# Kernel tuning notes

Hardware: AMD Instinct MI355X
Metric: run time of the kernel (lower is better)

Reference implementation:

```python
import jax, jax.numpy as jnp
import numpy as np

D_MODEL = 768
N_HEADS = 12
HEAD_DIM = D_MODEL // N_HEADS


def setup_inputs() -> dict:
    key = jax.random.key(0)
    ks = jax.random.split(key, 9)
    B, S = 4, 2048
    std = 1.0 / np.sqrt(D_MODEL)
    x = jax.random.normal(ks[0], (B, S, D_MODEL), dtype=jnp.float32)
    Wq = jax.random.normal(ks[1], (D_MODEL, D_MODEL), dtype=jnp.float32) * std
    bq = jnp.zeros((D_MODEL,), dtype=jnp.float32)
    Wk = jax.random.normal(ks[2], (D_MODEL, D_MODEL), dtype=jnp.float32) * std
    bk = jnp.zeros((D_MODEL,), dtype=jnp.float32)
    Wv = jax.random.normal(ks[3], (D_MODEL, D_MODEL), dtype=jnp.float32) * std
    bv = jnp.zeros((D_MODEL,), dtype=jnp.float32)
    Wo = jax.random.normal(ks[4], (D_MODEL, D_MODEL), dtype=jnp.float32) * std
    bo = jnp.zeros((D_MODEL,), dtype=jnp.float32)
    return {"x": x, "Wq": Wq, "bq": bq, "Wk": Wk, "bk": bk,
            "Wv": Wv, "bv": bv, "Wo": Wo, "bo": bo}


def reference(x, Wq, bq, Wk, bk, Wv, bv, Wo, bo):
    B, S, D = x.shape
    H, Hd = N_HEADS, HEAD_DIM
    # QKV projections (torch Linear: y = x @ W^T + b; here W stored as [in,out])
    q = (x @ Wq + bq).reshape(B, S, H, Hd).transpose(0, 2, 1, 3)  # [B,H,S,Hd]
    k = (x @ Wk + bk).reshape(B, S, H, Hd).transpose(0, 2, 1, 3)
    v = (x @ Wv + bv).reshape(B, S, H, Hd).transpose(0, 2, 1, 3)
    scale = 1.0 / jnp.sqrt(jnp.asarray(Hd, dtype=x.dtype))
    scores = jnp.einsum('bhqd,bhkd->bhqk', q, k) * scale  # [B,H,S,S]
    causal = jnp.tril(jnp.ones((S, S), dtype=bool))
    scores = jnp.where(causal, scores, -jnp.inf)
    attn = jax.nn.softmax(scores, axis=-1)
    ctx = jnp.einsum('bhqk,bhkd->bhqd', attn, v)  # [B,H,S,Hd]
    ctx = ctx.transpose(0, 2, 1, 3).reshape(B, S, D)
    return ctx @ Wo + bo
```

## Files before the change

### kernel.cpp

```cpp
#include <hip/hip_runtime.h>
#include <stdint.h>

#define DM    768
#define NH    12
#define HD    64
#define BATCH 4
#define SEQ   2048
#define NTOK  (BATCH*SEQ)
#define NKT   12

typedef unsigned int   u32;
typedef unsigned short u16;
using bf16x8 = __attribute__((ext_vector_type(8))) short;
using f32x4  = __attribute__((ext_vector_type(4))) float;

#define QSCALE 0.18033688011112042f

__device__ __forceinline__ u16 f2bf(float f) {
    u32 u = __float_as_uint(f);
    u = (u + 0x7FFFu + ((u >> 16) & 1u)) >> 16;
    return (u16)u;
}

__device__ __forceinline__ u32 pkbf(float a, float b) {
    u32 r;
    asm("v_cvt_pk_bf16_f32 %0, %1, %2" : "=v"(r) : "v"(a), "v"(b));
    return r;
}

template <int N>
__device__ __forceinline__ void waitvm() {
    if constexpr (N == 0)      asm volatile("s_waitcnt vmcnt(0)" ::: "memory");
    else if constexpr (N == 2) asm volatile("s_waitcnt vmcnt(2)" ::: "memory");
    else if constexpr (N == 4) asm volatile("s_waitcnt vmcnt(4)" ::: "memory");
    else if constexpr (N == 5) asm volatile("s_waitcnt vmcnt(5)" ::: "memory");
    else if constexpr (N == 8) asm volatile("s_waitcnt vmcnt(8)" ::: "memory");
    else if constexpr (N == 9) asm volatile("s_waitcnt vmcnt(9)" ::: "memory");
    else static_assert(N == 0 || N == 2 || N == 4 || N == 5 || N == 8 || N == 9, "add literal");
}

__device__ __forceinline__ void gload_lds16(const void* gptr, void* ldsptr) {
    __builtin_amdgcn_global_load_lds(
        (__attribute__((address_space(1))) const u32*)gptr,
        (__attribute__((address_space(3))) u32*)ldsptr, 16, 0, 0);
}

__device__ __forceinline__ float vmax4(f32x4 v) {
    return fmaxf(fmaxf(v[0], v[1]), fmaxf(v[2], v[3]));
}

__global__ void cvt_x(const float* __restrict__ x, u16* __restrict__ xb, int n4) {
    int i = blockIdx.x * blockDim.x + threadIdx.x;
    if (i >= n4) return;
    float4 v = ((const float4*)x)[i];
    ushort4 o;
    o.x = f2bf(v.x); o.y = f2bf(v.y); o.z = f2bf(v.z); o.w = f2bf(v.w);
    ((ushort4*)xb)[i] = o;
}

__global__ void transpose_w4(const float* __restrict__ q, const float* __restrict__ k,
                             const float* __restrict__ v, const float* __restrict__ o,
                             u16* __restrict__ Wt, u16* __restrict__ Wto) {
    __shared__ float tile[32][33];
    int z = blockIdx.z;
    const float* W = (z == 0) ? q : (z == 1) ? k : (z == 2) ? v : o;
    u16* D = (z < 3) ? (Wt + (size_t)z * DM * DM) : Wto;
    int tx = threadIdx.x, ty = threadIdx.y;
    int x0 = blockIdx.x * 32, y0 = blockIdx.y * 32;
    #pragma unroll
    for (int i = 0; i < 32; i += 8)
        tile[ty + i][tx] = W[(size_t)(y0 + ty + i) * DM + x0 + tx];
    __syncthreads();
    #pragma unroll
    for (int i = 0; i < 32; i += 8)
        D[(size_t)(x0 + ty + i) * DM + y0 + tx] = f2bf(tile[tx][ty + i]);
}

template <int MODE>
__global__ __launch_bounds__(512, 2)
void gemm_pipe(const u16* __restrict__ A, const u16* __restrict__ Bt,
               const float* __restrict__ b0, const float* __restrict__ b1,
               const float* __restrict__ b2,
               u16* __restrict__ Qo, u16* __restrict__ Ko, u16* __restrict__ Vto,
               float* __restrict__ Out)
{
    constexpr int BM = (MODE == 0) ? 256 : 128;
    constexpr int BN = (MODE == 0) ? 288 : 192;
    constexpr int MF = 4;
    constexpr int NF = (MODE == 0) ? 9 : 3;
    constexpr int AL = BM / 64;
    constexpr int BFULL = (MODE == 0) ? 4 : 3;

    __shared__ u16 As[2][BM][64];
    __shared__ u16 Bs[2][BN][64];

    const int t = threadIdx.x;
    const int w = t >> 6, l = t & 63;
    const int l15 = l & 15, lg = l >> 4;
    const int m0 = blockIdx.x * BM;
    const int n0 = blockIdx.y * BN;
    const int waveM = ((MODE == 0) ? (w >> 1) : (w >> 2)) * 64;
    const int waveN = (MODE == 0) ? (w & 1) * 144 : (w & 3) * 48;

    f32x4 zf = {0.f, 0.f, 0.f, 0.f};
    f32x4 acc[MF][NF];
    #pragma unroll
    for (int i = 0; i < MF; ++i)
        #pragma unroll
        for (int j = 0; j < NF; ++j) acc[i][j] = zf;

    const u16* Arow0 = A  + (size_t)m0 * DM;
    const u16* Brow0 = Bt + (size_t)n0 * DM;

    auto stage = [&](int d, int k0) {
        #pragma unroll
        for (int i = 0; i < AL; ++i) {
            int f = i * 512 + t;
            int row = f >> 3, c = f & 7;
            int gc = c ^ (row & 7);
            gload_lds16(Arow0 + (size_t)row * DM + k0 + gc * 8, &As[d][row][c * 8]);
        }
        #pragma unroll
        for (int i = 0; i < BFULL; ++i) {
            int f = i * 512 + t;
            int row = f >> 3, c = f & 7;
            int gc = c ^ (row & 7);
            gload_lds16(Brow0 + (size_t)row * DM + k0 + gc * 8, &Bs[d][row][c * 8]);
        }
        if constexpr (MODE == 0) {
            if (t < 256) {
                int f = 2048 + t;
                int row = f >> 3, c = f & 7;
                int gc = c ^ (row & 7);
                gload_lds16(Brow0 + (size_t)row * DM + k0 + gc * 8, &Bs[d][row][c * 8]);
            }
        }
    };
    auto wait_tile = [&]() {
        if constexpr (MODE == 0) {
            if (w < 4) waitvm<9>(); else waitvm<8>();
        } else {
            waitvm<5>();
        }
    };
    auto phase = [&](int d, int kk) {
        const int ch = ((kk * 4 + lg) ^ (l15 & 7)) * 8;
        bf16x8 af[MF], bfr[NF];
        #pragma unroll
        for (int m = 0; m < MF; ++m)
            af[m] = *(const bf16x8*)&As[d][waveM + m * 16 + l15][ch];
        #pragma unroll
        for (int n = 0; n < NF; ++n)
            bfr[n] = *(const bf16x8*)&Bs[d][waveN + n * 16 + l15][ch];
        __builtin_amdgcn_s_setprio(1);
        #pragma unroll
        for (int m = 0; m < MF; ++m)
            #pragma unroll
            for (int n = 0; n < NF; ++n)
                acc[m][n] = __builtin_amdgcn_mfma_f32_16x16x32_bf16(af[m], bfr[n], acc[m][n], 0, 0, 0);
        __builtin_amdgcn_s_setprio(0);
    };

    stage(0, 0);
    stage(1, 64);

    for (int tt = 0; tt < NKT - 1; ++tt) {
        const int c = tt & 1;
        wait_tile();
        __builtin_amdgcn_s_barrier();
        __builtin_amdgcn_sched_barrier(0);
        phase(c, 0);
        phase(c, 1);
        __builtin_amdgcn_sched_barrier(0);
        __builtin_amdgcn_s_barrier();
        __builtin_amdgcn_sched_barrier(0);
        if (tt + 2 < NKT) stage(c, (tt + 2) * 64);
    }
    {
        waitvm<0>();
        __builtin_amdgcn_s_barrier();
        __builtin_amdgcn_sched_barrier(0);
        phase((NKT - 1) & 1, 0);
        phase((NKT - 1) & 1, 1);
    }

    if (MODE == 1) {
        #pragma unroll
        for (int m = 0; m < MF; ++m) {
            int grow = m0 + waveM + m * 16 + lg * 4;
            #pragma unroll
            for (int n = 0; n < NF; ++n) {
                int gcol = n0 + waveN + n * 16 + l15;
                float bias = b0[gcol];
                #pragma unroll
                for (int r = 0; r < 4; ++r)
                    Out[(size_t)(grow + r) * DM + gcol] = acc[m][n][r] + bias;
            }
        }
    } else {
        #pragma unroll
        for (int m = 0; m < MF; ++m) {
            int grow = m0 + waveM + m * 16 + lg * 4;
            int bb = grow >> 11, ss = grow & 2047;
            #pragma unroll
            for (int n = 0; n < NF; ++n) {
                int nstart = n0 + waveN + n * 16;
                int which = nstart / DM;
                int cbase = nstart - which * DM + l15;
                int h = cbase >> 6, hd = cbase & 63;
                if (which == 0) {
                    float bias = b0[cbase];
                    #pragma unroll
                    for (int r = 0; r < 4; ++r)
                        Qo[(((size_t)bb * NH + h) * SEQ + (ss + r)) * HD + hd] =
                            f2bf((acc[m][n][r] + bias) * QSCALE);
                } else if (which == 1) {
                    float bias = b1[cbase];
                    #pragma unroll
                    for (int r = 0; r < 4; ++r)
                        Ko[(((size_t)bb * NH + h) * SEQ + (ss + r)) * HD + hd] =
                            f2bf(acc[m][n][r] + bias);
                } else {
                    float bias = b2[cbase];
                    u32 lo = pkbf(acc[m][n][0] + bias, acc[m][n][1] + bias);
                    u32 hi = pkbf(acc[m][n][2] + bias, acc[m][n][3] + bias);
                    *(int2*)&Vto[(((size_t)bb * NH + h) * HD + hd) * SEQ + ss] =
                        make_int2((int)lo, (int)hi);
                }
            }
        }
    }
}

__global__ __launch_bounds__(512, 4)
void attn_fwd(const u16* __restrict__ Q, const u16* __restrict__ K_,
              const u16* __restrict__ Vt, u16* __restrict__ ctx)
{
    __shared__ u16 Ks[2][64][64];
    __shared__ u16 Vs[2][64][64];

    const int t = threadIdx.x, w = t >> 6, l = t & 63;
    const int l15 = l & 15, lg = l >> 4;
    const int sw = l15 & 7;
    const int bx = blockIdx.x;
    const int ord = bx / 48;
    const int bh  = bx - ord * 48;
    const int q16 = 15 - ord;
    const int b = bh / NH, h = bh - b * NH;
    const int wrow0 = q16 * 128 + w * 16;
    const int niter = 2 * q16 + 2;

    const u16* Qp = Q + ((size_t)bh * SEQ + wrow0 + l15) * HD;
    bf16x8 qf0 = *(const bf16x8*)(Qp + lg * 8);
    bf16x8 qf1 = *(const bf16x8*)(Qp + 32 + lg * 8);

    f32x4 zf = {0.f, 0.f, 0.f, 0.f};
    f32x4 acc[4];
    #pragma unroll
    for (int d = 0; d < 4; ++d) acc[d] = zf;
    float mi = -INFINITY, li = 0.f;

    const u16* Kbh = K_ + (size_t)bh * SEQ * HD;
    const u16* Vbh = Vt + (size_t)bh * HD * SEQ;

    auto stage = [&](int d, int j0) {
        int row = t >> 3, c = t & 7;
        int gc = (c ^ (row & 7)) * 8;
        gload_lds16(Kbh + (size_t)(j0 + row) * HD + gc, (u16*)Ks[d] + (size_t)t * 8);
        gload_lds16(Vbh + (size_t)row * SEQ + j0 + gc,  (u16*)Vs[d] + (size_t)t * 8);
    };

    stage(0, 0);
    stage(1, 64);

    for (int jt = 0; jt < niter; ++jt) {
        const int cur = jt & 1;
        const int j0 = jt << 6;
        if (jt < niter - 1) waitvm<2>(); else waitvm<0>();
        __builtin_amdgcn_s_barrier();
        __builtin_amdgcn_sched_barrier(0);
        if (j0 <= wrow0 + 15) {
            const u16 (*Kc)[64] = Ks[cur];
            const u16 (*Vc)[64] = Vs[cur];
            f32x4 s0[4];
            __builtin_amdgcn_s_setprio(1);
            #pragma unroll
            for (int nt = 0; nt < 4; ++nt) {
                const u16* krow = Kc[nt * 16 + l15];
                bf16x8 kf0 = *(const bf16x8*)&krow[(lg ^ sw) * 8];
                bf16x8 kf1 = *(const bf16x8*)&krow[((4 + lg) ^ sw) * 8];
                f32x4 a = zf;
                a = __builtin_amdgcn_mfma_f32_16x16x32_bf16(kf0, qf0, a, 0, 0, 0);
                a = __builtin_amdgcn_mfma_f32_16x16x32_bf16(kf1, qf1, a, 0, 0, 0);
                s0[nt] = a;
            }
            __builtin_amdgcn_s_setprio(0);
            if (j0 + 63 > wrow0) {
                #pragma unroll
                for (int nt = 0; nt < 4; ++nt) {
                    int kb = j0 + nt * 16 + lg * 4;
                    #pragma unroll
                    for (int r = 0; r < 4; ++r)
                        if (kb + r > wrow0 + l15) s0[nt][r] = -INFINITY;
                }
            }
            float pm = fmaxf(fmaxf(vmax4(s0[0]), vmax4(s0[1])), fmaxf(vmax4(s0[2]), vmax4(s0[3])));
            pm = fmaxf(pm, __shfl_xor(pm, 16));
            pm = fmaxf(pm, __shfl_xor(pm, 32));
            if (!__all(pm <= mi + 8.f)) {
                float mn = fmaxf(mi, pm);
                float so = __builtin_amdgcn_exp2f(mi - mn);
                mi = mn;
                li *= so;
                float a0 = __shfl(so, lg * 4 + 0), a1 = __shfl(so, lg * 4 + 1);
                float a2 = __shfl(so, lg * 4 + 2), a3 = __shfl(so, lg * 4 + 3);
                #pragma unroll
                for (int d = 0; d < 4; ++d) {
                    acc[d][0] *= a0; acc[d][1] *= a1;
                    acc[d][2] *= a2; acc[d][3] *= a3;
                }
            }
            u32 dwa[8];
            float rs = 0.f;
            #pragma unroll
            for (int nt = 0; nt < 4; ++nt) {
                float p0 = __builtin_amdgcn_exp2f(s0[nt][0] - mi);
                float p1 = __builtin_amdgcn_exp2f(s0[nt][1] - mi);
                float p2 = __builtin_amdgcn_exp2f(s0[nt][2] - mi);
                float p3 = __builtin_amdgcn_exp2f(s0[nt][3] - mi);
                rs += (p0 + p1) + (p2 + p3);
                dwa[nt * 2] = pkbf(p0, p1); dwa[nt * 2 + 1] = pkbf(p2, p3);
            }
            rs += __shfl_xor(rs, 16);
            rs += __shfl_xor(rs, 32);
            li += rs;
            bf16x8 pa0 = __builtin_bit_cast(bf16x8, make_int4((int)dwa[0], (int)dwa[1], (int)dwa[2], (int)dwa[3]));
            bf16x8 pa1 = __builtin_bit_cast(bf16x8, make_int4((int)dwa[4], (int)dwa[5], (int)dwa[6], (int)dwa[7]));
            const int o4 = (lg & 1) * 4, c0 = lg >> 1;
            __builtin_amdgcn_s_setprio(1);
            #pragma unroll
            for (int d = 0; d < 4; ++d) {
                const u16* vrow = Vc[d * 16 + l15];
                int2 v0 = *(const int2*)(vrow + (((c0 + 0) ^ sw) * 8 + o4));
                int2 v1 = *(const int2*)(vrow + (((c0 + 2) ^ sw) * 8 + o4));
                int2 v2 = *(const int2*)(vrow + (((c0 + 4) ^ sw) * 8 + o4));
                int2 v3 = *(const int2*)(vrow + (((c0 + 6) ^ sw) * 8 + o4));
                bf16x8 vf0 = __builtin_bit_cast(bf16x8, make_int4(v0.x, v0.y, v1.x, v1.y));
                bf16x8 vf1 = __builtin_bit_cast(bf16x8, make_int4(v2.x, v2.y, v3.x, v3.y));
                acc[d] = __builtin_amdgcn_mfma_f32_16x16x32_bf16(pa0, vf0, acc[d], 0, 0, 0);
                acc[d] = __builtin_amdgcn_mfma_f32_16x16x32_bf16(pa1, vf1, acc[d], 0, 0, 0);
            }
            __builtin_amdgcn_s_setprio(0);
        }
        if (jt < niter - 1) {
            __builtin_amdgcn_s_barrier();
            __builtin_amdgcn_sched_barrier(0);
            if (jt + 2 < niter) stage(cur, (jt + 2) << 6);
        }
    }

    float e0 = 1.0f / __shfl(li, lg * 4 + 0), e1 = 1.0f / __shfl(li, lg * 4 + 1);
    float e2 = 1.0f / __shfl(li, lg * 4 + 2), e3 = 1.0f / __shfl(li, lg * 4 + 3);
    #pragma unroll
    for (int r = 0; r < 4; ++r) {
        float f0 = (r == 0) ? e0 : (r == 1) ? e1 : (r == 2) ? e2 : e3;
        int s = wrow0 + lg * 4 + r;
        size_t base = ((size_t)b * SEQ + s) * DM + h * HD;
        #pragma unroll
        for (int d = 0; d < 4; ++d)
            ctx[base + d * 16 + l15] = f2bf(acc[d][r] * f0);
    }
}

extern "C" void kernel_launch(void* const* d_in, const int* in_sizes, int n_in,
                              void* d_out, int out_size, void* d_ws, size_t ws_size,
                              hipStream_t stream) {
    const float* x  = (const float*)d_in[0];
    const float* Wq = (const float*)d_in[1];
    const float* bq = (const float*)d_in[2];
    const float* Wk = (const float*)d_in[3];
    const float* bk = (const float*)d_in[4];
    const float* Wv = (const float*)d_in[5];
    const float* bv = (const float*)d_in[6];
    const float* Wo = (const float*)d_in[7];
    const float* bo = (const float*)d_in[8];
    float* out = (float*)d_out;

    char* ws = (char*)d_ws;
    u16* xb  = (u16*)(ws);
    u16* Wt  = (u16*)(ws + 12582912);
    u16* Wto = (u16*)(ws + 16121856);
    u16* Qw  = (u16*)(ws + 17301504);
    u16* Kw  = (u16*)(ws + 29884416);
    u16* Vtw = (u16*)(ws + 42467328);
    u16* ctx = (u16*)(ws + 55050240);

    cvt_x<<<6144, 256, 0, stream>>>(x, xb, NTOK * DM / 4);
    dim3 tb(32, 8), tg4(24, 24, 4);
    transpose_w4<<<tg4, tb, 0, stream>>>(Wq, Wk, Wv, Wo, Wt, Wto);

    dim3 g2(32, 8);
    gemm_pipe<0><<<g2, 512, 0, stream>>>(xb, Wt, bq, bk, bv, Qw, Kw, Vtw, nullptr);
    attn_fwd<<<768, 512, 0, stream>>>(Qw, Kw, Vtw, ctx);
    dim3 g4(64, 4);
    gemm_pipe<1><<<g4, 512, 0, stream>>>(ctx, Wto, bo, nullptr, nullptr, nullptr, nullptr, nullptr, out);
}
```

Before: 124.9 us.

## Pair long and short causal query strips per block for load balance

Measured after the change: 124.8 us. Within noise of the previous version (-0.1%).

```diff
diff --git a/kernel.cpp b/kernel.cpp
--- a/kernel.cpp
+++ b/kernel.cpp
@@ -31,12 +31,11 @@
 template <int N>
 __device__ __forceinline__ void waitvm() {
     if constexpr (N == 0)      asm volatile("s_waitcnt vmcnt(0)" ::: "memory");
-    else if constexpr (N == 2) asm volatile("s_waitcnt vmcnt(2)" ::: "memory");
     else if constexpr (N == 4) asm volatile("s_waitcnt vmcnt(4)" ::: "memory");
     else if constexpr (N == 5) asm volatile("s_waitcnt vmcnt(5)" ::: "memory");
     else if constexpr (N == 8) asm volatile("s_waitcnt vmcnt(8)" ::: "memory");
     else if constexpr (N == 9) asm volatile("s_waitcnt vmcnt(9)" ::: "memory");
-    else static_assert(N == 0 || N == 2 || N == 4 || N == 5 || N == 8 || N == 9, "add literal");
+    else static_assert(N == 0 || N == 4 || N == 5 || N == 8 || N == 9, "add literal");
 }
 
 __device__ __forceinline__ void gload_lds16(const void* gptr, void* ldsptr) {
@@ -232,9 +231,8 @@
     }
 }
 
-__global__ __launch_bounds__(512, 4)
-void attn_fwd(const u16* __restrict__ Q, const u16* __restrict__ K_,
-              const u16* __restrict__ Vt, u16* __restrict__ ctx)
+__global__ void attn_fwd(const u16* __restrict__ Q, const u16* __restrict__ K_,
+                         const u16* __restrict__ Vt, u16* __restrict__ ctx)
 {
     __shared__ u16 Ks[2][64][64];
     __shared__ u16 Vs[2][64][64];
@@ -245,29 +243,113 @@
     const int bx = blockIdx.x;
     const int ord = bx / 48;
     const int bh  = bx - ord * 48;
-    const int q16 = 15 - ord;
+    const int qL = 31 - ord;
+    const int qS = ord;
     const int b = bh / NH, h = bh - b * NH;
-    const int wrow0 = q16 * 128 + w * 16;
-    const int niter = 2 * q16 + 2;
-
-    const u16* Qp = Q + ((size_t)bh * SEQ + wrow0 + l15) * HD;
-    bf16x8 qf0 = *(const bf16x8*)(Qp + lg * 8);
-    bf16x8 qf1 = *(const bf16x8*)(Qp + 32 + lg * 8);
+    const int wrowA = qL * 64 + w * 16;
+    const int wrowB = qS * 64 + w * 16;
+    const int niter = qL + 1;
+
+    const u16* QpA = Q + ((size_t)bh * SEQ + wrowA + l15) * HD;
+    const u16* QpB = Q + ((size_t)bh * SEQ + wrowB + l15) * HD;
+    bf16x8 qA0 = *(const bf16x8*)(QpA + lg * 8);
+    bf16x8 qA1 = *(const bf16x8*)(QpA + 32 + lg * 8);
+    bf16x8 qB0 = *(const bf16x8*)(QpB + lg * 8);
+    bf16x8 qB1 = *(const bf16x8*)(QpB + 32 + lg * 8);
 
     f32x4 zf = {0.f, 0.f, 0.f, 0.f};
-    f32x4 acc[4];
+    f32x4 accA[4], accB[4];
     #pragma unroll
-    for (int d = 0; d < 4; ++d) acc[d] = zf;
-    float mi = -INFINITY, li = 0.f;
+    for (int d = 0; d < 4; ++d) { accA[d] = zf; accB[d] = zf; }
+    float miA = -INFINITY, liA = 0.f;
+    float miB = -INFINITY, liB = 0.f;
 
     const u16* Kbh = K_ + (size_t)bh * SEQ * HD;
     const u16* Vbh = Vt + (size_t)bh * HD * SEQ;
 
     auto stage = [&](int d, int j0) {
-        int row = t >> 3, c = t & 7;
-        int gc = (c ^ (row & 7)) * 8;
-        gload_lds16(Kbh + (size_t)(j0 + row) * HD + gc, (u16*)Ks[d] + (size_t)t * 8);
-        gload_lds16(Vbh + (size_t)row * SEQ + j0 + gc,  (u16*)Vs[d] + (size_t)t * 8);
+        #pragma unroll
+        for (int i = 0; i < 2; ++i) {
+            int f = i * 256 + t;
+            int row = f >> 3, c = f & 7;
+            int gc = (c ^ (row & 7)) * 8;
+            gload_lds16(Kbh + (size_t)(j0 + row) * HD + gc, (u16*)Ks[d] + (size_t)f * 8);
+            gload_lds16(Vbh + (size_t)row * SEQ + j0 + gc,  (u16*)Vs[d] + (size_t)f * 8);
+        }
+    };
+
+    auto strip = [&](const bf16x8& q0, const bf16x8& q1, float& mi, float& li,
+                     f32x4 (&acc)[4], int wrow, bool diag,
+                     const u16 (*Kc)[64], const u16 (*Vc)[64], int j0) {
+        f32x4 s0[4];
+        __builtin_amdgcn_s_setprio(1);
+        #pragma unroll
+        for (int nt = 0; nt < 4; ++nt) {
+            const u16* krow = Kc[nt * 16 + l15];
+            bf16x8 kf0 = *(const bf16x8*)&krow[(lg ^ sw) * 8];
+            bf16x8 kf1 = *(const bf16x8*)&krow[((4 + lg) ^ sw) * 8];
+            f32x4 a = zf;
+            a = __builtin_amdgcn_mfma_f32_16x16x32_bf16(kf0, q0, a, 0, 0, 0);
+            a = __builtin_amdgcn_mfma_f32_16x16x32_bf16(kf1, q1, a, 0, 0, 0);
+            s0[nt] = a;
+        }
+        __builtin_amdgcn_s_setprio(0);
+        if (diag) {
+            #pragma unroll
+            for (int nt = 0; nt < 4; ++nt) {
+                int kb = j0 + nt * 16 + lg * 4;
+                #pragma unroll
+                for (int r = 0; r < 4; ++r)
+                    if (kb + r > wrow + l15) s0[nt][r] = -INFINITY;
+            }
+        }
+        float pm = fmaxf(fmaxf(vmax4(s0[0]), vmax4(s0[1])), fmaxf(vmax4(s0[2]), vmax4(s0[3])));
+        pm = fmaxf(pm, __shfl_xor(pm, 16));
+        pm = fmaxf(pm, __shfl_xor(pm, 32));
+        if (!__all(pm <= mi + 8.f)) {
+            float mn = fmaxf(mi, pm);
+            float so = __builtin_amdgcn_exp2f(mi - mn);
+            mi = mn;
+            li *= so;
+            float a0 = __shfl(so, lg * 4 + 0), a1 = __shfl(so, lg * 4 + 1);
+            float a2 = __shfl(so, lg * 4 + 2), a3 = __shfl(so, lg * 4 + 3);
+            #pragma unroll
+            for (int d = 0; d < 4; ++d) {
+                acc[d][0] *= a0; acc[d][1] *= a1;
+                acc[d][2] *= a2; acc[d][3] *= a3;
+            }
+        }
+        u32 dwa[8];
+        float rs = 0.f;
+        #pragma unroll
+        for (int nt = 0; nt < 4; ++nt) {
+            float p0 = __builtin_amdgcn_exp2f(s0[nt][0] - mi);
+            float p1 = __builtin_amdgcn_exp2f(s0[nt][1] - mi);
+            float p2 = __builtin_amdgcn_exp2f(s0[nt][2] - mi);
+            float p3 = __builtin_amdgcn_exp2f(s0[nt][3] - mi);
+            rs += (p0 + p1) + (p2 + p3);
+            dwa[nt * 2] = pkbf(p0, p1); dwa[nt * 2 + 1] = pkbf(p2, p3);
+        }
+        rs += __shfl_xor(rs, 16);
+        rs += __shfl_xor(rs, 32);
+        li += rs;
+        bf16x8 pa0 = __builtin_bit_cast(bf16x8, make_int4((int)dwa[0], (int)dwa[1], (int)dwa[2], (int)dwa[3]));
+        bf16x8 pa1 = __builtin_bit_cast(bf16x8, make_int4((int)dwa[4], (int)dwa[5], (int)dwa[6], (int)dwa[7]));
+        const int o4 = (lg & 1) * 4, c0 = lg >> 1;
+        __builtin_amdgcn_s_setprio(1);
+        #pragma unroll
+        for (int d = 0; d < 4; ++d) {
+            const u16* vrow = Vc[d * 16 + l15];
+            int2 v0 = *(const int2*)(vrow + (((c0 + 0) ^ sw) * 8 + o4));
+            int2 v1 = *(const int2*)(vrow + (((c0 + 2) ^ sw) * 8 + o4));
+            int2 v2 = *(const int2*)(vrow + (((c0 + 4) ^ sw) * 8 + o4));
+            int2 v3 = *(const int2*)(vrow + (((c0 + 6) ^ sw) * 8 + o4));
+            bf16x8 vf0 = __builtin_bit_cast(bf16x8, make_int4(v0.x, v0.y, v1.x, v1.y));
+            bf16x8 vf1 = __builtin_bit_cast(bf16x8, make_int4(v2.x, v2.y, v3.x, v3.y));
+            acc[d] = __builtin_amdgcn_mfma_f32_16x16x32_bf16(pa0, vf0, acc[d], 0, 0, 0);
+            acc[d] = __builtin_amdgcn_mfma_f32_16x16x32_bf16(pa1, vf1, acc[d], 0, 0, 0);
+        }
+        __builtin_amdgcn_s_setprio(0);
     };
 
     stage(0, 0);
@@ -276,82 +358,12 @@
     for (int jt = 0; jt < niter; ++jt) {
         const int cur = jt & 1;
         const int j0 = jt << 6;
-        if (jt < niter - 1) waitvm<2>(); else waitvm<0>();
+        if (jt < niter - 1) waitvm<4>(); else waitvm<0>();
         __builtin_amdgcn_s_barrier();
         __builtin_amdgcn_sched_barrier(0);
-        if (j0 <= wrow0 + 15) {
-            const u16 (*Kc)[64] = Ks[cur];
-            const u16 (*Vc)[64] = Vs[cur];
-            f32x4 s0[4];
-            __builtin_amdgcn_s_setprio(1);
-            #pragma unroll
-            for (int nt = 0; nt < 4; ++nt) {
-                const u16* krow = Kc[nt * 16 + l15];
-                bf16x8 kf0 = *(const bf16x8*)&krow[(lg ^ sw) * 8];
-                bf16x8 kf1 = *(const bf16x8*)&krow[((4 + lg) ^ sw) * 8];
-                f32x4 a = zf;
-                a = __builtin_amdgcn_mfma_f32_16x16x32_bf16(kf0, qf0, a, 0, 0, 0);
-                a = __builtin_amdgcn_mfma_f32_16x16x32_bf16(kf1, qf1, a, 0, 0, 0);
-                s0[nt] = a;
-            }
-            __builtin_amdgcn_s_setprio(0);
-            if (j0 + 63 > wrow0) {
-                #pragma unroll
-                for (int nt = 0; nt < 4; ++nt) {
-                    int kb = j0 + nt * 16 + lg * 4;
-                    #pragma unroll
-                    for (int r = 0; r < 4; ++r)
-                        if (kb + r > wrow0 + l15) s0[nt][r] = -INFINITY;
-                }
-            }
-            float pm = fmaxf(fmaxf(vmax4(s0[0]), vmax4(s0[1])), fmaxf(vmax4(s0[2]), vmax4(s0[3])));
-            pm = fmaxf(pm, __shfl_xor(pm, 16));
-            pm = fmaxf(pm, __shfl_xor(pm, 32));
-            if (!__all(pm <= mi + 8.f)) {
-                float mn = fmaxf(mi, pm);
-                float so = __builtin_amdgcn_exp2f(mi - mn);
-                mi = mn;
-                li *= so;
-                float a0 = __shfl(so, lg * 4 + 0), a1 = __shfl(so, lg * 4 + 1);
-                float a2 = __shfl(so, lg * 4 + 2), a3 = __shfl(so, lg * 4 + 3);
-                #pragma unroll
-                for (int d = 0; d < 4; ++d) {
-                    acc[d][0] *= a0; acc[d][1] *= a1;
-                    acc[d][2] *= a2; acc[d][3] *= a3;
-                }
-            }
-            u32 dwa[8];
-            float rs = 0.f;
-            #pragma unroll
-            for (int nt = 0; nt < 4; ++nt) {
-                float p0 = __builtin_amdgcn_exp2f(s0[nt][0] - mi);
-                float p1 = __builtin_amdgcn_exp2f(s0[nt][1] - mi);
-                float p2 = __builtin_amdgcn_exp2f(s0[nt][2] - mi);
-                float p3 = __builtin_amdgcn_exp2f(s0[nt][3] - mi);
-                rs += (p0 + p1) + (p2 + p3);
-                dwa[nt * 2] = pkbf(p0, p1); dwa[nt * 2 + 1] = pkbf(p2, p3);
-            }
-            rs += __shfl_xor(rs, 16);
-            rs += __shfl_xor(rs, 32);
-            li += rs;
-            bf16x8 pa0 = __builtin_bit_cast(bf16x8, make_int4((int)dwa[0], (int)dwa[1], (int)dwa[2], (int)dwa[3]));
-            bf16x8 pa1 = __builtin_bit_cast(bf16x8, make_int4((int)dwa[4], (int)dwa[5], (int)dwa[6], (int)dwa[7]));
-            const int o4 = (lg & 1) * 4, c0 = lg >> 1;
-            __builtin_amdgcn_s_setprio(1);
-            #pragma unroll
-            for (int d = 0; d < 4; ++d) {
-                const u16* vrow = Vc[d * 16 + l15];
-                int2 v0 = *(const int2*)(vrow + (((c0 + 0) ^ sw) * 8 + o4));
-                int2 v1 = *(const int2*)(vrow + (((c0 + 2) ^ sw) * 8 + o4));
-                int2 v2 = *(const int2*)(vrow + (((c0 + 4) ^ sw) * 8 + o4));
-                int2 v3 = *(const int2*)(vrow + (((c0 + 6) ^ sw) * 8 + o4));
-                bf16x8 vf0 = __builtin_bit_cast(bf16x8, make_int4(v0.x, v0.y, v1.x, v1.y));
-                bf16x8 vf1 = __builtin_bit_cast(bf16x8, make_int4(v2.x, v2.y, v3.x, v3.y));
-                acc[d] = __builtin_amdgcn_mfma_f32_16x16x32_bf16(pa0, vf0, acc[d], 0, 0, 0);
-                acc[d] = __builtin_amdgcn_mfma_f32_16x16x32_bf16(pa1, vf1, acc[d], 0, 0, 0);
-            }
-            __builtin_amdgcn_s_setprio(0);
-        }
+        strip(qA0, qA1, miA, liA, accA, wrowA, jt == qL, Ks[cur], Vs[cur], j0);
+        if (jt <= qS)
+            strip(qB0, qB1, miB, liB, accB, wrowB, jt == qS, Ks[cur], Vs[cur], j0);
         if (jt < niter - 1) {
             __builtin_amdgcn_s_barrier();
             __builtin_amdgcn_sched_barrier(0);
@@ -359,17 +371,21 @@
         }
     }
 
-    float e0 = 1.0f / __shfl(li, lg * 4 + 0), e1 = 1.0f / __shfl(li, lg * 4 + 1);
-    float e2 = 1.0f / __shfl(li, lg * 4 + 2), e3 = 1.0f / __shfl(li, lg * 4 + 3);
-    #pragma unroll
-    for (int r = 0; r < 4; ++r) {
-        float f0 = (r == 0) ? e0 : (r == 1) ? e1 : (r == 2) ? e2 : e3;
-        int s = wrow0 + lg * 4 + r;
-        size_t base = ((size_t)b * SEQ + s) * DM + h * HD;
-        #pragma unroll
-        for (int d = 0; d < 4; ++d)
-            ctx[base + d * 16 + l15] = f2bf(acc[d][r] * f0);
-    }
+    auto epi = [&](float li, f32x4 (&acc)[4], int wrow) {
+        float e0 = 1.0f / __shfl(li, lg * 4 + 0), e1 = 1.0f / __shfl(li, lg * 4 + 1);
+        float e2 = 1.0f / __shfl(li, lg * 4 + 2), e3 = 1.0f / __shfl(li, lg * 4 + 3);
+        #pragma unroll
+        for (int r = 0; r < 4; ++r) {
+            float f0 = (r == 0) ? e0 : (r == 1) ? e1 : (r == 2) ? e2 : e3;
+            int s = wrow + lg * 4 + r;
+            size_t base = ((size_t)b * SEQ + s) * DM + h * HD;
+            #pragma unroll
+            for (int d = 0; d < 4; ++d)
+                ctx[base + d * 16 + l15] = f2bf(acc[d][r] * f0);
+        }
+    };
+    epi(liA, accA, wrowA);
+    epi(liB, accB, wrowB);
 }
 
 extern "C" void kernel_launch(void* const* d_in, const int* in_sizes, int n_in,
@@ -401,7 +417,7 @@
 
     dim3 g2(32, 8);
     gemm_pipe<0><<<g2, 512, 0, stream>>>(xb, Wt, bq, bk, bv, Qw, Kw, Vtw, nullptr);
-    attn_fwd<<<768, 512, 0, stream>>>(Qw, Kw, Vtw, ctx);
+    attn_fwd<<<768, 256, 0, stream>>>(Qw, Kw, Vtw, ctx);
     dim3 g4(64, 4);
     gemm_pipe<1><<<g4, 512, 0, stream>>>(ctx, Wto, bo, nullptr, nullptr, nullptr, nullptr, nullptr, out);
 }
```
